# Kernel optimization log

Hardware: AMD Instinct MI355X
Metric: run time of the kernel (lower is better)

Reference implementation:

```python
import jax, jax.numpy as jnp
import numpy as np

N = 50000
E = 800000
DES, TW, NUMP, CATP = 768, 768, 4, 3
EMB = 384
THIRD = EMB // 3  # 128


def _lin(key, fan_in, fan_out):
    k1, k2 = jax.random.split(key)
    bound = 1.0 / np.sqrt(fan_in)
    W = jax.random.uniform(k1, (fan_in, fan_out), jnp.float32, -bound, bound)
    b = jax.random.uniform(k2, (fan_out,), jnp.float32, -bound, bound)
    return W, b


def setup_inputs() -> dict:
    key = jax.random.key(0)
    ks = jax.random.split(key, 16)
    des = jax.random.normal(ks[0], (N, DES), jnp.float32)
    tweet = jax.random.normal(ks[1], (N, TW), jnp.float32)
    num_prop = jax.random.normal(ks[2], (N, NUMP), jnp.float32)
    cat_prop = jax.random.normal(ks[3], (N, CATP), jnp.float32)
    edge_index = jax.random.randint(ks[4], (2, E), 0, N, jnp.int64)
    W_des, b_des = _lin(ks[5], DES, THIRD)
    W_num, b_num = _lin(ks[6], NUMP, THIRD)
    W_cat, b_cat = _lin(ks[7], CATP, THIRD)
    W_in, b_in = _lin(ks[8], EMB, EMB)
    W_g1, b_g1 = _lin(ks[9], EMB, EMB)
    W_g2, b_g2 = _lin(ks[10], EMB, EMB)
    W_o1, b_o1 = _lin(ks[11], EMB, EMB)
    W_o2, b_o2 = _lin(ks[12], EMB, 2)
    return dict(des=des, tweet=tweet, num_prop=num_prop, cat_prop=cat_prop,
                edge_index=edge_index,
                W_des=W_des, b_des=b_des, W_num=W_num, b_num=b_num,
                W_cat=W_cat, b_cat=b_cat, W_in=W_in, b_in=b_in,
                W_g1=W_g1, b_g1=b_g1, W_g2=W_g2, b_g2=b_g2,
                W_o1=W_o1, b_o1=b_o1, W_o2=W_o2, b_o2=b_o2)


def _leaky(x):
    return jax.nn.leaky_relu(x, 0.01)


def _gcn_conv(x, edge_index, W, b):
    # PyG GCNConv: x' = D^{-1/2} (A + I) D^{-1/2} (x W) + b
    src, dst = edge_index[0], edge_index[1]
    x = x @ W  # [N, out]
    n = x.shape[0]
    deg = jax.ops.segment_sum(jnp.ones(src.shape[0], x.dtype), dst, num_segments=n) + 1.0  # self-loop
    dinv = jax.lax.rsqrt(deg)  # deg >= 1
    norm = dinv[src] * dinv[dst]  # [E]
    msg = x[src] * norm[:, None]  # [E, out] gather
    agg = jax.ops.segment_sum(msg, dst, num_segments=n)  # scatter-add
    agg = agg + x * (dinv * dinv)[:, None]  # self-loop contribution
    return agg + b


def reference(des, tweet, num_prop, cat_prop, edge_index,
              W_des, b_des, W_num, b_num, W_cat, b_cat, W_in, b_in,
              W_g1, b_g1, W_g2, b_g2, W_o1, b_o1, W_o2, b_o2):
    # eval mode: dropout is identity
    d = _leaky(des @ W_des + b_des)
    n = _leaky(num_prop @ W_num + b_num)
    c = _leaky(cat_prop @ W_cat + b_cat)
    x = jnp.concatenate((d, n, c), axis=1)  # [N, EMB]
    x = _leaky(x @ W_in + b_in)
    x = _gcn_conv(x, edge_index, W_g1, b_g1)
    x = _gcn_conv(x, edge_index, W_g2, b_g2)
    x = _leaky(x @ W_o1 + b_o1)
    return x @ W_o2 + b_o2  # [N, 2]
```

## Files before the change

### kernel.cpp

```cpp
#include <hip/hip_runtime.h>
#include <hip/hip_bf16.h>
#include <cstdint>

#define NFEAT 384
#define DESK 768
#define THIRD 128

typedef __bf16 bf16x8 __attribute__((ext_vector_type(8)));
typedef unsigned short u16x8 __attribute__((ext_vector_type(8)));
typedef unsigned short u16x4 __attribute__((ext_vector_type(4)));
typedef float f32x16 __attribute__((ext_vector_type(16)));
typedef _Float16 h16x2 __attribute__((ext_vector_type(2)));

__device__ __forceinline__ float leaky(float x) { return x > 0.f ? x : 0.01f * x; }

__device__ __forceinline__ unsigned short bfhi(float x) {
  unsigned int u = __float_as_uint(x);
  u += 0x7fffu + ((u >> 16) & 1u);
  return (unsigned short)(u >> 16);
}
__device__ __forceinline__ float bf2f(unsigned short h) {
  return __uint_as_float(((unsigned int)h) << 16);
}
__device__ __forceinline__ void bsplit(float x, unsigned short& h,
                                       unsigned short& l) {
  h = bfhi(x);
  l = bfhi(x - bf2f(h));
}

#define MFMA(a, b, c) __builtin_amdgcn_mfma_f32_32x32x16_bf16(a, b, c, 0, 0, 0)

template <int AFP32, int EPI>
__global__ __launch_bounds__(256, 2) void mfma_gemm(
    const float* __restrict__ Af, const unsigned short* __restrict__ Ahi,
    const unsigned short* __restrict__ Alo,
    const unsigned short* __restrict__ BThi,
    const unsigned short* __restrict__ BTlo, _Float16* __restrict__ Ch16,
    unsigned short* __restrict__ Chi, unsigned short* __restrict__ Clo,
    const float* __restrict__ bias, int M, int K, int ldc) {
  __shared__ unsigned short AhiL[4 * 128 * 8];
  __shared__ unsigned short AloL[4 * 128 * 8];
  __shared__ unsigned short BhiL[4 * 128 * 8];
  __shared__ unsigned short BloL[4 * 128 * 8];
  const int tid = threadIdx.x;
  const int lane = tid & 63;
  const int w = tid >> 6;
  const int wm = (w >> 1) * 64, wn = (w & 1) * 64;
  const int lm = lane & 31, lk = lane >> 5;
  const int m_base = blockIdx.x * 128, n_base = blockIdx.y * 128;
  f32x16 a00 = {0.f, 0.f, 0.f, 0.f, 0.f, 0.f, 0.f, 0.f,
                0.f, 0.f, 0.f, 0.f, 0.f, 0.f, 0.f, 0.f};
  f32x16 a01 = a00, a10 = a00, a11 = a00;

  for (int kt = 0; kt < K; kt += 32) {
    if (AFP32) {
#pragma unroll
      for (int it = 0; it < 4; it++) {
        int r = (tid >> 3) + it * 32;
        int q = tid & 7;
        int gr = m_base + r;
        float4 av = make_float4(0.f, 0.f, 0.f, 0.f);
        if (gr < M) av = *(const float4*)&Af[(size_t)gr * K + kt + q * 4];
        unsigned short h0, h1, h2, h3, l0, l1, l2, l3;
        bsplit(av.x, h0, l0);
        bsplit(av.y, h1, l1);
        bsplit(av.z, h2, l2);
        bsplit(av.w, h3, l3);
        int base = ((q >> 1) * 128 + r) * 8 + (q & 1) * 4;
        u16x4 th;
        th.x = h0; th.y = h1; th.z = h2; th.w = h3;
        u16x4 tl;
        tl.x = l0; tl.y = l1; tl.z = l2; tl.w = l3;
        *(u16x4*)&AhiL[base] = th;
        *(u16x4*)&AloL[base] = tl;
      }
    } else {
#pragma unroll
      for (int it = 0; it < 2; it++) {
        int r = (tid >> 2) + it * 64;
        int kb = tid & 3;
        int gr = m_base + r;
        u16x8 vh = {0, 0, 0, 0, 0, 0, 0, 0};
        u16x8 vl = {0, 0, 0, 0, 0, 0, 0, 0};
        if (gr < M) {
          vh = *(const u16x8*)&Ahi[(size_t)gr * K + kt + kb * 8];
          vl = *(const u16x8*)&Alo[(size_t)gr * K + kt + kb * 8];
        }
        *(u16x8*)&AhiL[(kb * 128 + r) * 8] = vh;
        *(u16x8*)&AloL[(kb * 128 + r) * 8] = vl;
      }
    }
#pragma unroll
    for (int it = 0; it < 2; it++) {
      int n = (tid >> 2) + it * 64;
      int kb = tid & 3;
      *(u16x8*)&BhiL[(kb * 128 + n) * 8] =
          *(const u16x8*)&BThi[(size_t)(n_base + n) * K + kt + kb * 8];
      *(u16x8*)&BloL[(kb * 128 + n) * 8] =
          *(const u16x8*)&BTlo[(size_t)(n_base + n) * K + kt + kb * 8];
    }
    __syncthreads();
#pragma unroll
    for (int ks = 0; ks < 2; ks++) {
      int kb = 2 * ks + lk;
      bf16x8 ah0 = __builtin_bit_cast(
          bf16x8, *(const u16x8*)&AhiL[(kb * 128 + wm + lm) * 8]);
      bf16x8 ah1 = __builtin_bit_cast(
          bf16x8, *(const u16x8*)&AhiL[(kb * 128 + wm + 32 + lm) * 8]);
      bf16x8 al0 = __builtin_bit_cast(
          bf16x8, *(const u16x8*)&AloL[(kb * 128 + wm + lm) * 8]);
      bf16x8 al1 = __builtin_bit_cast(
          bf16x8, *(const u16x8*)&AloL[(kb * 128 + wm + 32 + lm) * 8]);
      bf16x8 bh0 = __builtin_bit_cast(
          bf16x8, *(const u16x8*)&BhiL[(kb * 128 + wn + lm) * 8]);
      bf16x8 bh1 = __builtin_bit_cast(
          bf16x8, *(const u16x8*)&BhiL[(kb * 128 + wn + 32 + lm) * 8]);
      bf16x8 bl0 = __builtin_bit_cast(
          bf16x8, *(const u16x8*)&BloL[(kb * 128 + wn + lm) * 8]);
      bf16x8 bl1 = __builtin_bit_cast(
          bf16x8, *(const u16x8*)&BloL[(kb * 128 + wn + 32 + lm) * 8]);
      a00 = MFMA(ah0, bh0, a00);
      a01 = MFMA(ah0, bh1, a01);
      a10 = MFMA(ah1, bh0, a10);
      a11 = MFMA(ah1, bh1, a11);
      a00 = MFMA(ah0, bl0, a00);
      a01 = MFMA(ah0, bl1, a01);
      a10 = MFMA(ah1, bl0, a10);
      a11 = MFMA(ah1, bl1, a11);
      a00 = MFMA(al0, bh0, a00);
      a01 = MFMA(al0, bh1, a01);
      a10 = MFMA(al1, bh0, a10);
      a11 = MFMA(al1, bh1, a11);
    }
    __syncthreads();
  }
  const int colb = n_base + wn;
#pragma unroll
  for (int mt = 0; mt < 2; mt++) {
#pragma unroll
    for (int nt = 0; nt < 2; nt++) {
      f32x16 v = (mt == 0) ? (nt == 0 ? a00 : a01) : (nt == 0 ? a10 : a11);
      int col = colb + nt * 32 + lm;
      float bv = (EPI == 0) ? bias[col] : 0.f;
      int rb = m_base + wm + mt * 32 + 4 * lk;
#pragma unroll
      for (int rg = 0; rg < 16; rg++) {
        int row = rb + (rg & 3) + 8 * (rg >> 2);
        if (row < M) {
          float x = v[rg];
          if (EPI == 0) {
            x = leaky(x + bv);
            unsigned short h, l;
            bsplit(x, h, l);
            Chi[(size_t)row * ldc + col] = h;
            Clo[(size_t)row * ldc + col] = l;
          } else {
            Ch16[(size_t)row * ldc + col] = (_Float16)x;
          }
        }
      }
    }
  }
}

__global__ __launch_bounds__(256) void split_transpose_b(
    const float* __restrict__ s0, unsigned short* __restrict__ h0,
    unsigned short* __restrict__ l0, const float* __restrict__ s1,
    unsigned short* __restrict__ h1, unsigned short* __restrict__ l1,
    const float* __restrict__ s2, unsigned short* __restrict__ h2,
    unsigned short* __restrict__ l2) {
  int z = blockIdx.z;
  const float* src = z == 0 ? s0 : (z == 1 ? s1 : s2);
  unsigned short* dsthi = z == 0 ? h0 : (z == 1 ? h1 : h2);
  unsigned short* dstlo = z == 0 ? l0 : (z == 1 ? l1 : l2);
  int R = z == 0 ? 768 : 384;
  int C = z == 0 ? 128 : 384;
  int c0 = blockIdx.x * 32, r0 = blockIdx.y * 32;
  if (c0 >= C || r0 >= R) return;
  __shared__ float tile[32][33];
  int tx = threadIdx.x & 31, ty = threadIdx.x >> 5;
#pragma unroll
  for (int i = 0; i < 4; i++)
    tile[ty + i * 8][tx] = src[(size_t)(r0 + ty + i * 8) * C + c0 + tx];
  __syncthreads();
#pragma unroll
  for (int i = 0; i < 4; i++) {
    int c = c0 + ty + i * 8, r = r0 + tx;
    float v = tile[tx][ty + i * 8];
    unsigned short h, l;
    bsplit(v, h, l);
    dsthi[(size_t)c * R + r] = h;
    dstlo[(size_t)c * R + r] = l;
  }
}

__global__ __launch_bounds__(256) void gemm384(const float* __restrict__ A,
                                               const float* __restrict__ B,
                                               float* __restrict__ C) {
  __shared__ float As[16][68];
  __shared__ float Bs[16][64];
  const int tid = threadIdx.x;
  const int mb = blockIdx.x * 64;
  const int nb = blockIdx.y * 64;
  float acc[4][4] = {};
  const int arow = tid >> 2, akq = tid & 3;
  const int brow = tid >> 4, bc4 = tid & 15;
  const int m0 = (tid >> 4) * 4, n0 = (tid & 15) * 4;
  for (int kk = 0; kk < 384; kk += 16) {
    float4 av = *(const float4*)&A[(mb + arow) * 384 + kk + akq * 4];
    As[akq * 4 + 0][arow] = av.x;
    As[akq * 4 + 1][arow] = av.y;
    As[akq * 4 + 2][arow] = av.z;
    As[akq * 4 + 3][arow] = av.w;
    *(float4*)&Bs[brow][bc4 * 4] =
        *(const float4*)&B[(kk + brow) * 384 + nb + bc4 * 4];
    __syncthreads();
#pragma unroll
    for (int k = 0; k < 16; k++) {
      float4 a4 = *(const float4*)&As[k][m0];
      float4 b4 = *(const float4*)&Bs[k][n0];
      float a[4] = {a4.x, a4.y, a4.z, a4.w};
      float b[4] = {b4.x, b4.y, b4.z, b4.w};
#pragma unroll
      for (int i = 0; i < 4; i++)
#pragma unroll
        for (int j = 0; j < 4; j++) acc[i][j] = fmaf(a[i], b[j], acc[i][j]);
    }
    __syncthreads();
  }
#pragma unroll
  for (int i = 0; i < 4; i++)
#pragma unroll
    for (int j = 0; j < 4; j++)
      C[(mb + m0 + i) * 384 + nb + n0 + j] = acc[i][j];
}

__global__ void uv_kernel(const float* __restrict__ T1,
                          const float* __restrict__ W_o1,
                          const float* __restrict__ b_g1,
                          const float* __restrict__ b_g2,
                          const float* __restrict__ b_o1, float* __restrict__ u,
                          float* __restrict__ v) {
  int j = blockIdx.x * blockDim.x + threadIdx.x;
  if (j < 384) {
    float su = 0.f, sv = 0.f;
    for (int k = 0; k < 384; k++) {
      su = fmaf(T1[k * 384 + j], b_g1[k], su);
      sv = fmaf(W_o1[k * 384 + j], b_g2[k], sv);
    }
    u[j] = su;
    v[j] = sv + b_o1[j];
  }
}

__global__ __launch_bounds__(256) void numcat_kernel(
    const float* __restrict__ num, const float* __restrict__ cat,
    const float* __restrict__ Wn, const float* __restrict__ bn,
    const float* __restrict__ Wc, const float* __restrict__ bc,
    unsigned short* __restrict__ x0hi, unsigned short* __restrict__ x0lo,
    int N) {
  int c = threadIdx.x;
  for (int i = blockIdx.x; i < N; i += gridDim.x) {
    float val;
    if (c < 128) {
      val = bn[c];
      val = fmaf(num[i * 4 + 0], Wn[0 * 128 + c], val);
      val = fmaf(num[i * 4 + 1], Wn[1 * 128 + c], val);
      val = fmaf(num[i * 4 + 2], Wn[2 * 128 + c], val);
      val = fmaf(num[i * 4 + 3], Wn[3 * 128 + c], val);
    } else {
      int cc = c - 128;
      val = bc[cc];
      val = fmaf(cat[i * 3 + 0], Wc[0 * 128 + cc], val);
      val = fmaf(cat[i * 3 + 1], Wc[1 * 128 + cc], val);
      val = fmaf(cat[i * 3 + 2], Wc[2 * 128 + cc], val);
    }
    val = leaky(val);
    unsigned short h, l;
    bsplit(val, h, l);
    size_t o = (size_t)i * NFEAT + 128 + c;
    x0hi[o] = h;
    x0lo[o] = l;
  }
}

__global__ void count_kernel(const int* __restrict__ dst, int* __restrict__ deg,
                             int E) {
  int e = blockIdx.x * blockDim.x + threadIdx.x;
  if (e < E) atomicAdd(&deg[dst[e]], 1);
}

__global__ void scan_reduce(const int* __restrict__ deg,
                            int* __restrict__ partial, int N) {
  __shared__ int sm[512];
  int i = blockIdx.x * 512 + threadIdx.x;
  sm[threadIdx.x] = (i < N) ? deg[i] : 0;
  __syncthreads();
  for (int off = 256; off; off >>= 1) {
    if (threadIdx.x < off) sm[threadIdx.x] += sm[threadIdx.x + off];
    __syncthreads();
  }
  if (threadIdx.x == 0) partial[blockIdx.x] = sm[0];
}

__global__ void scan_top(int* partial, int nb) {
  if (threadIdx.x == 0 && blockIdx.x == 0) {
    int run = 0;
    for (int b = 0; b < nb; b++) {
      int t = partial[b];
      partial[b] = run;
      run += t;
    }
  }
}

__global__ void scan_down(const int* __restrict__ deg,
                          const int* __restrict__ partial,
                          int* __restrict__ offsets, int* __restrict__ cursor,
                          float* __restrict__ dinv, int N, int E) {
  __shared__ int sm[512];
  int t = threadIdx.x;
  int i = blockIdx.x * 512 + t;
  int val = (i < N) ? deg[i] : 0;
  sm[t] = val;
  __syncthreads();
  for (int off = 1; off < 512; off <<= 1) {
    int add = (t >= off) ? sm[t - off] : 0;
    __syncthreads();
    sm[t] += add;
    __syncthreads();
  }
  if (i < N) {
    int ex = partial[blockIdx.x] + sm[t] - val;
    offsets[i] = ex;
    cursor[i] = ex;
    dinv[i] = 1.0f / sqrtf((float)val + 1.0f);
  }
  if (i == 0) offsets[N] = E;
}

__global__ void fill_kernel(const int* __restrict__ src,
                            const int* __restrict__ dst,
                            int* __restrict__ cursor,
                            int* __restrict__ csr_off,
                            float* __restrict__ csr_w,
                            const float* __restrict__ dinv, int E) {
  int e = blockIdx.x * blockDim.x + threadIdx.x;
  if (e < E) {
    int s = src[e], d = dst[e];
    int slot = atomicAdd(&cursor[d], 1);
    csr_off[slot] = s * NFEAT;
    csr_w[slot] = dinv[s] * dinv[d];
  }
}

template <int WRITE_S, int FINAL>
__global__ __launch_bounds__(192) void agg_kernel(
    const _Float16* __restrict__ xin, _Float16* __restrict__ xout,
    const int* __restrict__ offsets, const int* __restrict__ csr_off,
    const float* __restrict__ csr_w, const float* __restrict__ dinv,
    float* __restrict__ sout, const float* __restrict__ svec,
    const float* __restrict__ uvec, const float* __restrict__ vvec,
    const float* __restrict__ W_o2, const float* __restrict__ b_o2,
    float* __restrict__ out, int N) {
  const int t = threadIdx.x;
  const int ff = 2 * t;
  __shared__ int ssrc[192];
  __shared__ float sw[192];
  __shared__ float red[3][2];
  float u0 = 0.f, u1 = 0.f, vc0 = 0.f, vc1 = 0.f;
  float w00 = 0.f, w01 = 0.f, w10 = 0.f, w11 = 0.f, bo0 = 0.f, bo1 = 0.f;
  if (FINAL) {
    u0 = uvec[ff];
    u1 = uvec[ff + 1];
    vc0 = vvec[ff];
    vc1 = vvec[ff + 1];
    w00 = W_o2[ff * 2 + 0];
    w01 = W_o2[ff * 2 + 1];
    w10 = W_o2[(ff + 1) * 2 + 0];
    w11 = W_o2[(ff + 1) * 2 + 1];
    bo0 = b_o2[0];
    bo1 = b_o2[1];
  }
  for (int i = blockIdx.x; i < N; i += gridDim.x) {
    int beg = offsets[i], end = offsets[i + 1];
    float di = dinv[i];
    float dii = di * di;
    h16x2 xs = *(const h16x2*)&xin[(size_t)i * NFEAT + ff];
    float A0x = dii * (float)xs.x, A0y = dii * (float)xs.y;
    float A1x = 0.f, A1y = 0.f, A2x = 0.f, A2y = 0.f, A3x = 0.f, A3y = 0.f;
    float wsum = dii;
    for (int j0 = beg; j0 < end; j0 += 192) {
      int cnt = min(192, end - j0);
      if (t < cnt) {
        ssrc[t] = csr_off[j0 + t];
        sw[t] = csr_w[j0 + t];
      }
      __syncthreads();
      int j = 0;
      for (; j + 8 <= cnt; j += 8) {
        int o0 = ssrc[j + 0], o1 = ssrc[j + 1], o2 = ssrc[j + 2],
            o3 = ssrc[j + 3];
        int o4 = ssrc[j + 4], o5 = ssrc[j + 5], o6 = ssrc[j + 6],
            o7 = ssrc[j + 7];
        float w0 = sw[j + 0], w1 = sw[j + 1], w2 = sw[j + 2], w3 = sw[j + 3];
        float w4 = sw[j + 4], w5 = sw[j + 5], w6 = sw[j + 6], w7 = sw[j + 7];
        h16x2 v0 = *(const h16x2*)&xin[o0 + ff];
        h16x2 v1 = *(const h16x2*)&xin[o1 + ff];
        h16x2 v2 = *(const h16x2*)&xin[o2 + ff];
        h16x2 v3 = *(const h16x2*)&xin[o3 + ff];
        h16x2 v4 = *(const h16x2*)&xin[o4 + ff];
        h16x2 v5 = *(const h16x2*)&xin[o5 + ff];
        h16x2 v6 = *(const h16x2*)&xin[o6 + ff];
        h16x2 v7 = *(const h16x2*)&xin[o7 + ff];
        A0x = fmaf(w0, (float)v0.x, A0x);
        A0y = fmaf(w0, (float)v0.y, A0y);
        A1x = fmaf(w1, (float)v1.x, A1x);
        A1y = fmaf(w1, (float)v1.y, A1y);
        A2x = fmaf(w2, (float)v2.x, A2x);
        A2y = fmaf(w2, (float)v2.y, A2y);
        A3x = fmaf(w3, (float)v3.x, A3x);
        A3y = fmaf(w3, (float)v3.y, A3y);
        A0x = fmaf(w4, (float)v4.x, A0x);
        A0y = fmaf(w4, (float)v4.y, A0y);
        A1x = fmaf(w5, (float)v5.x, A1x);
        A1y = fmaf(w5, (float)v5.y, A1y);
        A2x = fmaf(w6, (float)v6.x, A2x);
        A2y = fmaf(w6, (float)v6.y, A2y);
        A3x = fmaf(w7, (float)v7.x, A3x);
        A3y = fmaf(w7, (float)v7.y, A3y);
        if (WRITE_S) wsum += ((w0 + w1) + (w2 + w3)) + ((w4 + w5) + (w6 + w7));
      }
      for (; j < cnt; j++) {
        float wj = sw[j];
        h16x2 vj = *(const h16x2*)&xin[ssrc[j] + ff];
        A0x = fmaf(wj, (float)vj.x, A0x);
        A0y = fmaf(wj, (float)vj.y, A0y);
        if (WRITE_S) wsum += wj;
      }
      __syncthreads();
    }
    float ax = (A0x + A1x) + (A2x + A3x);
    float ay = (A0y + A1y) + (A2y + A3y);
    if (!FINAL) {
      h16x2 r;
      r.x = (_Float16)ax;
      r.y = (_Float16)ay;
      *(h16x2*)&xout[(size_t)i * NFEAT + ff] = r;
      if (WRITE_S && t == 0) sout[i] = wsum;
    } else {
      float si = svec[i];
      float q0 = leaky(ax + si * u0 + vc0);
      float q1 = leaky(ay + si * u1 + vc1);
      float c0 = q0 * w00 + q1 * w10;
      float c1 = q0 * w01 + q1 * w11;
#pragma unroll
      for (int off2 = 32; off2; off2 >>= 1) {
        c0 += __shfl_down(c0, off2, 64);
        c1 += __shfl_down(c1, off2, 64);
      }
      int wid = t >> 6, lane2 = t & 63;
      if (lane2 == 0) {
        red[wid][0] = c0;
        red[wid][1] = c1;
      }
      __syncthreads();
      if (t == 0) {
        out[i * 2 + 0] = red[0][0] + red[1][0] + red[2][0] + bo0;
        out[i * 2 + 1] = red[0][1] + red[1][1] + red[2][1] + bo1;
      }
    }
  }
}

extern "C" void kernel_launch(void* const* d_in, const int* in_sizes, int n_in,
                              void* d_out, int out_size, void* d_ws,
                              size_t ws_size, hipStream_t stream) {
  const float* des = (const float*)d_in[0];
  const float* num_prop = (const float*)d_in[2];
  const float* cat_prop = (const float*)d_in[3];
  const int* edge = (const int*)d_in[4];
  const float* W_des = (const float*)d_in[5];
  const float* b_des = (const float*)d_in[6];
  const float* W_num = (const float*)d_in[7];
  const float* b_num = (const float*)d_in[8];
  const float* W_cat = (const float*)d_in[9];
  const float* b_cat = (const float*)d_in[10];
  const float* W_in = (const float*)d_in[11];
  const float* b_in = (const float*)d_in[12];
  const float* W_g1 = (const float*)d_in[13];
  const float* b_g1 = (const float*)d_in[14];
  const float* W_g2 = (const float*)d_in[15];
  const float* b_g2 = (const float*)d_in[16];
  const float* W_o1 = (const float*)d_in[17];
  const float* b_o1 = (const float*)d_in[18];
  const float* W_o2 = (const float*)d_in[19];
  const float* b_o2 = (const float*)d_in[20];
  float* out = (float*)d_out;

  const int N = in_sizes[0] / DESK;
  const int E = in_sizes[4] / 2;
  const int* esrc = edge;
  const int* edst = edge + E;

  char* ws = (char*)d_ws;
  size_t off = 0;
  auto alloc = [&](size_t n) {
    off = (off + 255) & ~(size_t)255;
    size_t o = off;
    off += n;
    return o;
  };
  float* bufA = (float*)(ws + alloc((size_t)N * NFEAT * 4));
  float* bufB = (float*)(ws + alloc((size_t)N * NFEAT * 4));
  int* deg = (int*)(ws + alloc((size_t)N * 4));
  int* offsets = (int*)(ws + alloc((size_t)(N + 1) * 4));
  int* cursor = (int*)(ws + alloc((size_t)N * 4));
  int* partial = (int*)(ws + alloc(1024 * 4));
  float* dinv = (float*)(ws + alloc((size_t)N * 4));
  float* svec = (float*)(ws + alloc((size_t)N * 4));
  int* csr_off = (int*)(ws + alloc((size_t)E * 4));
  float* csr_w = (float*)(ws + alloc((size_t)E * 4));
  float* T1 = (float*)(ws + alloc(384 * 384 * 4));
  float* Mmat = (float*)(ws + alloc(384 * 384 * 4));
  float* uvec = (float*)(ws + alloc(384 * 4));
  float* vvec = (float*)(ws + alloc(384 * 4));
  unsigned short* WdThi = (unsigned short*)(ws + alloc(768 * 128 * 2));
  unsigned short* WdTlo = (unsigned short*)(ws + alloc(768 * 128 * 2));
  unsigned short* WiThi = (unsigned short*)(ws + alloc(384 * 384 * 2));
  unsigned short* WiTlo = (unsigned short*)(ws + alloc(384 * 384 * 2));
  unsigned short* MmThi = (unsigned short*)(ws + alloc(384 * 384 * 2));
  unsigned short* MmTlo = (unsigned short*)(ws + alloc(384 * 384 * 2));
  (void)ws_size;
  (void)n_in;
  (void)out_size;

  unsigned short* x0hi = (unsigned short*)bufA;
  unsigned short* x0lo = x0hi + (size_t)N * NFEAT;
  unsigned short* x1hi = (unsigned short*)bufB;
  unsigned short* x1lo = x1hi + (size_t)N * NFEAT;
  _Float16* yb = (_Float16*)bufA;
  _Float16* w1 = (_Float16*)bufB;

  hipMemsetAsync(deg, 0, (size_t)N * 4, stream);

  dim3 g6(6, 6);
  gemm384<<<g6, 256, 0, stream>>>(W_g2, W_o1, T1);
  gemm384<<<g6, 256, 0, stream>>>(W_g1, T1, Mmat);
  uv_kernel<<<2, 256, 0, stream>>>(T1, W_o1, b_g1, b_g2, b_o1, uvec, vvec);
  split_transpose_b<<<dim3(12, 24, 3), 256, 0, stream>>>(
      W_des, WdThi, WdTlo, W_in, WiThi, WiTlo, Mmat, MmThi, MmTlo);

  const int MT = (N + 127) / 128;
  mfma_gemm<1, 0><<<dim3(MT, 1), 256, 0, stream>>>(
      des, nullptr, nullptr, WdThi, WdTlo, nullptr, x0hi, x0lo, b_des, N, DESK,
      NFEAT);
  numcat_kernel<<<1024, 256, 0, stream>>>(num_prop, cat_prop, W_num, b_num,
                                          W_cat, b_cat, x0hi, x0lo, N);
  mfma_gemm<0, 0><<<dim3(MT, 3), 256, 0, stream>>>(
      nullptr, x0hi, x0lo, WiThi, WiTlo, nullptr, x1hi, x1lo, b_in, N, NFEAT,
      NFEAT);
  mfma_gemm<0, 1><<<dim3(MT, 3), 256, 0, stream>>>(
      nullptr, x1hi, x1lo, MmThi, MmTlo, yb, nullptr, nullptr, nullptr, N,
      NFEAT, NFEAT);

  const int EB = (E + 255) / 256;
  count_kernel<<<EB, 256, 0, stream>>>(edst, deg, E);
  const int NB = (N + 511) / 512;
  scan_reduce<<<NB, 512, 0, stream>>>(deg, partial, N);
  scan_top<<<1, 64, 0, stream>>>(partial, NB);
  scan_down<<<NB, 512, 0, stream>>>(deg, partial, offsets, cursor, dinv, N, E);
  fill_kernel<<<EB, 256, 0, stream>>>(esrc, edst, cursor, csr_off, csr_w, dinv,
                                      E);

  agg_kernel<1, 0><<<4096, 192, 0, stream>>>(
      yb, w1, offsets, csr_off, csr_w, dinv, svec, nullptr, nullptr, nullptr,
      nullptr, nullptr, nullptr, N);
  agg_kernel<0, 1><<<4096, 192, 0, stream>>>(
      w1, nullptr, offsets, csr_off, csr_w, dinv, nullptr, svec, uvec, vvec,
      W_o2, b_o2, out, N);
}
```

Measured before the change: 947.5 us.

## Prefetch next GEMM K-tile into registers and shrink des GEMM M-tile

The MFMA GEMM now loads the next K-slice of A and B into registers while the current slice is being computed from LDS, so global load latency overlaps with the matrix math. The tile height becomes a template parameter, and the des projection GEMM (768-wide K, only one N-tile) uses 64-row tiles. That doubles its block count to fill more compute units. The cost is more live registers for the prefetch buffers, which may reduce occupancy, and less B reuse per block in the smaller-tile GEMM.

```diff
diff --git a/kernel.cpp b/kernel.cpp
--- a/kernel.cpp
+++ b/kernel.cpp
@@ -30,7 +30,7 @@
 
 #define MFMA(a, b, c) __builtin_amdgcn_mfma_f32_32x32x16_bf16(a, b, c, 0, 0, 0)
 
-template <int AFP32, int EPI>
+template <int AFP32, int EPI, int BM>
 __global__ __launch_bounds__(256, 2) void mfma_gemm(
     const float* __restrict__ Af, const unsigned short* __restrict__ Ahi,
     const unsigned short* __restrict__ Alo,
@@ -38,35 +38,80 @@
     const unsigned short* __restrict__ BTlo, _Float16* __restrict__ Ch16,
     unsigned short* __restrict__ Chi, unsigned short* __restrict__ Clo,
     const float* __restrict__ bias, int M, int K, int ldc) {
-  __shared__ unsigned short AhiL[4 * 128 * 8];
-  __shared__ unsigned short AloL[4 * 128 * 8];
+  __shared__ unsigned short AhiL[4 * BM * 8];
+  __shared__ unsigned short AloL[4 * BM * 8];
   __shared__ unsigned short BhiL[4 * 128 * 8];
   __shared__ unsigned short BloL[4 * 128 * 8];
   const int tid = threadIdx.x;
   const int lane = tid & 63;
   const int w = tid >> 6;
-  const int wm = (w >> 1) * 64, wn = (w & 1) * 64;
+  constexpr int MR = BM / 64;
+  const int wm = (w >> 1) * (BM / 2);
+  const int wn = (w & 1) * 64;
   const int lm = lane & 31, lk = lane >> 5;
-  const int m_base = blockIdx.x * 128, n_base = blockIdx.y * 128;
-  f32x16 a00 = {0.f, 0.f, 0.f, 0.f, 0.f, 0.f, 0.f, 0.f,
-                0.f, 0.f, 0.f, 0.f, 0.f, 0.f, 0.f, 0.f};
-  f32x16 a01 = a00, a10 = a00, a11 = a00;
-
-  for (int kt = 0; kt < K; kt += 32) {
+  const int m_base = blockIdx.x * BM, n_base = blockIdx.y * 128;
+
+  f32x16 acc[MR][2];
+#pragma unroll
+  for (int mi = 0; mi < MR; mi++)
+#pragma unroll
+    for (int nt = 0; nt < 2; nt++)
+#pragma unroll
+      for (int r = 0; r < 16; r++) acc[mi][nt][r] = 0.f;
+
+  constexpr int AIT_F = BM / 32;
+  constexpr int AIT_H = BM / 64;
+  float4 pa[AIT_F];
+  u16x8 pah[AIT_H], pal[AIT_H];
+  u16x8 pbh[2], pbl[2];
+
+  auto loadA = [&](int kt) {
     if (AFP32) {
 #pragma unroll
-      for (int it = 0; it < 4; it++) {
+      for (int it = 0; it < AIT_F; it++) {
+        int r = (tid >> 3) + it * 32;
+        int gr = m_base + r;
+        float4 av = make_float4(0.f, 0.f, 0.f, 0.f);
+        if (gr < M) av = *(const float4*)&Af[(size_t)gr * K + kt + (tid & 7) * 4];
+        pa[it] = av;
+      }
+    } else {
+#pragma unroll
+      for (int it = 0; it < AIT_H; it++) {
+        int r = (tid >> 2) + it * 64;
+        int gr = m_base + r;
+        u16x8 vh = {0, 0, 0, 0, 0, 0, 0, 0};
+        u16x8 vl = {0, 0, 0, 0, 0, 0, 0, 0};
+        if (gr < M) {
+          vh = *(const u16x8*)&Ahi[(size_t)gr * K + kt + (tid & 3) * 8];
+          vl = *(const u16x8*)&Alo[(size_t)gr * K + kt + (tid & 3) * 8];
+        }
+        pah[it] = vh;
+        pal[it] = vl;
+      }
+    }
+  };
+  auto loadB = [&](int kt) {
+#pragma unroll
+    for (int it = 0; it < 2; it++) {
+      int n = (tid >> 2) + it * 64;
+      pbh[it] = *(const u16x8*)&BThi[(size_t)(n_base + n) * K + kt + (tid & 3) * 8];
+      pbl[it] = *(const u16x8*)&BTlo[(size_t)(n_base + n) * K + kt + (tid & 3) * 8];
+    }
+  };
+  auto storeLDS = [&]() {
+    if (AFP32) {
+#pragma unroll
+      for (int it = 0; it < AIT_F; it++) {
         int r = (tid >> 3) + it * 32;
         int q = tid & 7;
-        int gr = m_base + r;
-        float4 av = make_float4(0.f, 0.f, 0.f, 0.f);
-        if (gr < M) av = *(const float4*)&Af[(size_t)gr * K + kt + q * 4];
+        float4 av = pa[it];
         unsigned short h0, h1, h2, h3, l0, l1, l2, l3;
         bsplit(av.x, h0, l0);
         bsplit(av.y, h1, l1);
         bsplit(av.z, h2, l2);
         bsplit(av.w, h3, l3);
-        int base = ((q >> 1) * 128 + r) * 8 + (q & 1) * 4;
+        int base = ((q >> 1) * BM + r) * 8 + (q & 1) * 4;
         u16x4 th;
         th.x = h0; th.y = h1; th.z = h2; th.w = h3;
         u16x4 tl;
@@ -76,41 +121,42 @@
       }
     } else {
 #pragma unroll
-      for (int it = 0; it < 2; it++) {
+      for (int it = 0; it < AIT_H; it++) {
         int r = (tid >> 2) + it * 64;
         int kb = tid & 3;
-        int gr = m_base + r;
-        u16x8 vh = {0, 0, 0, 0, 0, 0, 0, 0};
-        u16x8 vl = {0, 0, 0, 0, 0, 0, 0, 0};
-        if (gr < M) {
-          vh = *(const u16x8*)&Ahi[(size_t)gr * K + kt + kb * 8];
-          vl = *(const u16x8*)&Alo[(size_t)gr * K + kt + kb * 8];
-        }
-        *(u16x8*)&AhiL[(kb * 128 + r) * 8] = vh;
-        *(u16x8*)&AloL[(kb * 128 + r) * 8] = vl;
+        *(u16x8*)&AhiL[(kb * BM + r) * 8] = pah[it];
+        *(u16x8*)&AloL[(kb * BM + r) * 8] = pal[it];
       }
     }
 #pragma unroll
     for (int it = 0; it < 2; it++) {
       int n = (tid >> 2) + it * 64;
       int kb = tid & 3;
-      *(u16x8*)&BhiL[(kb * 128 + n) * 8] =
-          *(const u16x8*)&BThi[(size_t)(n_base + n) * K + kt + kb * 8];
-      *(u16x8*)&BloL[(kb * 128 + n) * 8] =
-          *(const u16x8*)&BTlo[(size_t)(n_base + n) * K + kt + kb * 8];
-    }
+      *(u16x8*)&BhiL[(kb * 128 + n) * 8] = pbh[it];
+      *(u16x8*)&BloL[(kb * 128 + n) * 8] = pbl[it];
+    }
+  };
+
+  loadA(0);
+  loadB(0);
+  for (int kt = 0; kt < K; kt += 32) {
+    storeLDS();
     __syncthreads();
+    if (kt + 32 < K) {
+      loadA(kt + 32);
+      loadB(kt + 32);
+    }
 #pragma unroll
     for (int ks = 0; ks < 2; ks++) {
       int kb = 2 * ks + lk;
-      bf16x8 ah0 = __builtin_bit_cast(
-          bf16x8, *(const u16x8*)&AhiL[(kb * 128 + wm + lm) * 8]);
-      bf16x8 ah1 = __builtin_bit_cast(
-          bf16x8, *(const u16x8*)&AhiL[(kb * 128 + wm + 32 + lm) * 8]);
-      bf16x8 al0 = __builtin_bit_cast(
-          bf16x8, *(const u16x8*)&AloL[(kb * 128 + wm + lm) * 8]);
-      bf16x8 al1 = __builtin_bit_cast(
-          bf16x8, *(const u16x8*)&AloL[(kb * 128 + wm + 32 + lm) * 8]);
+      bf16x8 ah[MR], al[MR];
+#pragma unroll
+      for (int mi = 0; mi < MR; mi++) {
+        ah[mi] = __builtin_bit_cast(
+            bf16x8, *(const u16x8*)&AhiL[(kb * BM + wm + mi * 32 + lm) * 8]);
+        al[mi] = __builtin_bit_cast(
+            bf16x8, *(const u16x8*)&AloL[(kb * BM + wm + mi * 32 + lm) * 8]);
+      }
       bf16x8 bh0 = __builtin_bit_cast(
           bf16x8, *(const u16x8*)&BhiL[(kb * 128 + wn + lm) * 8]);
       bf16x8 bh1 = __builtin_bit_cast(
@@ -119,30 +165,27 @@
           bf16x8, *(const u16x8*)&BloL[(kb * 128 + wn + lm) * 8]);
       bf16x8 bl1 = __builtin_bit_cast(
           bf16x8, *(const u16x8*)&BloL[(kb * 128 + wn + 32 + lm) * 8]);
-      a00 = MFMA(ah0, bh0, a00);
-      a01 = MFMA(ah0, bh1, a01);
-      a10 = MFMA(ah1, bh0, a10);
-      a11 = MFMA(ah1, bh1, a11);
-      a00 = MFMA(ah0, bl0, a00);
-      a01 = MFMA(ah0, bl1, a01);
-      a10 = MFMA(ah1, bl0, a10);
-      a11 = MFMA(ah1, bl1, a11);
-      a00 = MFMA(al0, bh0, a00);
-      a01 = MFMA(al0, bh1, a01);
-      a10 = MFMA(al1, bh0, a10);
-      a11 = MFMA(al1, bh1, a11);
+#pragma unroll
+      for (int mi = 0; mi < MR; mi++) {
+        acc[mi][0] = MFMA(ah[mi], bh0, acc[mi][0]);
+        acc[mi][1] = MFMA(ah[mi], bh1, acc[mi][1]);
+        acc[mi][0] = MFMA(ah[mi], bl0, acc[mi][0]);
+        acc[mi][1] = MFMA(ah[mi], bl1, acc[mi][1]);
+        acc[mi][0] = MFMA(al[mi], bh0, acc[mi][0]);
+        acc[mi][1] = MFMA(al[mi], bh1, acc[mi][1]);
+      }
     }
     __syncthreads();
   }
   const int colb = n_base + wn;
 #pragma unroll
-  for (int mt = 0; mt < 2; mt++) {
+  for (int mi = 0; mi < MR; mi++) {
 #pragma unroll
     for (int nt = 0; nt < 2; nt++) {
-      f32x16 v = (mt == 0) ? (nt == 0 ? a00 : a01) : (nt == 0 ? a10 : a11);
+      f32x16 v = acc[mi][nt];
       int col = colb + nt * 32 + lm;
       float bv = (EPI == 0) ? bias[col] : 0.f;
-      int rb = m_base + wm + mt * 32 + 4 * lk;
+      int rb = m_base + wm + mi * 32 + 4 * lk;
 #pragma unroll
       for (int rg = 0; rg < 16; rg++) {
         int row = rb + (rg & 3) + 8 * (rg >> 2);
@@ -552,15 +595,16 @@
       W_des, WdThi, WdTlo, W_in, WiThi, WiTlo, Mmat, MmThi, MmTlo);
 
   const int MT = (N + 127) / 128;
-  mfma_gemm<1, 0><<<dim3(MT, 1), 256, 0, stream>>>(
+  const int MT64 = (N + 63) / 64;
+  mfma_gemm<1, 0, 64><<<dim3(MT64, 1), 256, 0, stream>>>(
       des, nullptr, nullptr, WdThi, WdTlo, nullptr, x0hi, x0lo, b_des, N, DESK,
       NFEAT);
   numcat_kernel<<<1024, 256, 0, stream>>>(num_prop, cat_prop, W_num, b_num,
                                           W_cat, b_cat, x0hi, x0lo, N);
-  mfma_gemm<0, 0><<<dim3(MT, 3), 256, 0, stream>>>(
+  mfma_gemm<0, 0, 128><<<dim3(MT, 3), 256, 0, stream>>>(
       nullptr, x0hi, x0lo, WiThi, WiTlo, nullptr, x1hi, x1lo, b_in, N, NFEAT,
       NFEAT);
-  mfma_gemm<0, 1><<<dim3(MT, 3), 256, 0, stream>>>(
+  mfma_gemm<0, 1, 128><<<dim3(MT, 3), 256, 0, stream>>>(
       nullptr, x1hi, x1lo, MmThi, MmTlo, yb, nullptr, nullptr, nullptr, N,
       NFEAT, NFEAT);
 
```

After: 911.3 us. 3.8% less time.
